# Kernel optimization log

Hardware: AMD Instinct MI355X
Metric: run time of the kernel (lower is better)

The kernel has to match this reference:

```python
import jax, jax.numpy as jnp
import numpy as np

N, S, P, F = 128, 32, 16, 256   # agents, samples, processes, encoder dim
H, NH = 4, 128                  # heads, n_hidden (is_concat=False -> n_hidden=out_features)
SLOPE = 0.2


def setup_inputs() -> dict:
    key = jax.random.key(0)
    k1, k2, k3, k4 = jax.random.split(key, 4)
    h = jax.random.normal(k1, (N, S, P, F), dtype=jnp.float32)
    W_l = jax.random.normal(k2, (F, H * NH), dtype=jnp.float32) / np.float32(np.sqrt(F))
    W_r = jax.random.normal(k3, (F, H * NH), dtype=jnp.float32) / np.float32(np.sqrt(F))
    attn_w = jax.random.normal(k4, (2 * NH,), dtype=jnp.float32) / np.float32(np.sqrt(2 * NH))
    return {"h": h, "W_l": W_l, "W_r": W_r, "attn_w": attn_w}


def reference(h, W_l, W_r, attn_w):
    n, s, p, f = h.shape
    hp = jnp.transpose(h, (1, 2, 0, 3))                 # [S,P,N,F]
    g_l = (hp @ W_l).reshape(s, p, n, H, NH)            # [S,P,N,H,NH]
    g_r = (hp @ W_r).reshape(s, p, n, H, NH)
    # attn(concat(gl[j], gr[i])) == <gl[j], a_l> + <gr[i], a_r>
    a_l, a_r = attn_w[:NH], attn_w[NH:]
    score_l = jnp.einsum('spnhf,f->spnh', g_l, a_l)     # contributes along j
    score_r = jnp.einsum('spnhf,f->spnh', g_r, a_r)     # contributes along i
    e = score_r[:, :, :, None, :] + score_l[:, :, None, :, :]   # [S,P,i,j,H]
    e = jnp.where(e >= 0, e, SLOPE * e)                 # LeakyReLU
    diag = jnp.eye(n, dtype=bool)[None, None, :, :, None]
    e = jnp.where(diag, -jnp.inf, e)                    # mask self-attention
    a = jax.nn.softmax(e, axis=3)                       # softmax over j
    out = jnp.einsum('spijh,spjhf->spihf', a, g_r)      # [S,P,N,H,NH]
    out = out.mean(axis=3)                              # is_concat=False -> mean over heads
    out = jnp.transpose(out, (2, 0, 1, 3))              # [N,S,P,NH]
    return out, a
```

## Files before the change

### kernel.cpp

```cpp
#include <hip/hip_runtime.h>
#include <hip/hip_bf16.h>

#define DI __device__ __forceinline__

namespace {
constexpr int N_ = 128, S_ = 32, P_ = 16, F_ = 256, H_ = 4, NH_ = 128;
constexpr int SP_ = S_ * P_;
constexpr int ROWS_ = N_ * SP_;
constexpr int GC_ = H_ * NH_;
constexpr float SLOPE_ = 0.2f;
constexpr int OUT_ELEMS = N_ * SP_ * NH_;
}

DI float lrelu(float x) { return x >= 0.f ? x : SLOPE_ * x; }

DI unsigned short f2h(float x) {
    _Float16 h = (_Float16)x;
    return __builtin_bit_cast(unsigned short, h);
}
DI float h2f(unsigned short b) {
    return (float)__builtin_bit_cast(_Float16, b);
}

typedef __fp16   fp16x2 __attribute__((ext_vector_type(2)));
typedef _Float16 f16x8 __attribute__((ext_vector_type(8)));
typedef float    f32x4 __attribute__((ext_vector_type(4)));

DI unsigned int pk2(float a, float b) {
    fp16x2 r = __builtin_amdgcn_cvt_pkrtz(a, b);
    return __builtin_bit_cast(unsigned int, r);
}

DI f32x4 mfma16h(uint4 a, uint4 b, f32x4 c) {
    return __builtin_amdgcn_mfma_f32_16x16x32_f16(
        __builtin_bit_cast(f16x8, a), __builtin_bit_cast(f16x8, b), c, 0, 0, 0);
}

__global__ __launch_bounds__(256) void prep_kernel(
    const float* __restrict__ Wl, const float* __restrict__ Wr,
    const float* __restrict__ aw, float* __restrict__ wls, float* __restrict__ wrs) {
    int t = blockIdx.x * 256 + threadIdx.x;
    int which = t >> 10;
    int f = (t & 1023) >> 2;
    int h = t & 3;
    const float* W = which ? Wr : Wl;
    const float* a = aw + which * NH_;
    const float* wrow = W + (size_t)f * GC_ + h * NH_;
    float s = 0.f;
    for (int k = 0; k < NH_; ++k) s += wrow[k] * a[k];
    (which ? wrs : wls)[f * H_ + h] = s;
}

__global__ __launch_bounds__(256) void prep_bt(
    const float* __restrict__ Wr, unsigned short* __restrict__ bth,
    unsigned short* __restrict__ btl) {
    int t = blockIdx.x * 256 + threadIdx.x;
    int col = t >> 5, k0 = (t & 31) * 8;
    union { unsigned short us[8]; uint4 v; } ph, pl;
#pragma unroll
    for (int e = 0; e < 8; ++e) {
        float v = Wr[(size_t)(k0 + e) * GC_ + col] * 256.0f;
        unsigned short hi = f2h(v);
        ph.us[e] = hi;
        pl.us[e] = f2h(v - h2f(hi));
    }
    *(uint4*)&bth[col * F_ + k0] = ph.v;
    *(uint4*)&btl[col * F_ + k0] = pl.v;
}

__global__ __launch_bounds__(256) void score_kernel(
    const float* __restrict__ hm, const float* __restrict__ wls,
    const float* __restrict__ wrs, float* __restrict__ sl, float* __restrict__ sr) {
    int r = blockIdx.x * 256 + threadIdx.x;
    const float4* hr  = (const float4*)(hm + (size_t)r * F_);
    const float4* wl4 = (const float4*)wls;
    const float4* wr4 = (const float4*)wrs;
    float4 al = {0.f,0.f,0.f,0.f}, ar = {0.f,0.f,0.f,0.f};
    for (int f0 = 0; f0 < F_; f0 += 4) {
        float4 hv = hr[f0 >> 2];
        float hx[4] = {hv.x, hv.y, hv.z, hv.w};
#pragma unroll
        for (int u = 0; u < 4; ++u) {
            float4 wl = wl4[f0 + u], wr = wr4[f0 + u];
            al.x += hx[u] * wl.x; al.y += hx[u] * wl.y;
            al.z += hx[u] * wl.z; al.w += hx[u] * wl.w;
            ar.x += hx[u] * wr.x; ar.y += hx[u] * wr.y;
            ar.z += hx[u] * wr.z; ar.w += hx[u] * wr.w;
        }
    }
    int n = r >> 9, sp = r & 511;
    ((float4*)sl)[sp * N_ + n] = al;
    ((float4*)sr)[sp * N_ + n] = ar;
}

__global__ __launch_bounds__(512, 2) void gat_fused(
    const float* __restrict__ sl_g, const float* __restrict__ sr_g,
    const float* __restrict__ hm,
    const unsigned short* __restrict__ bth, const unsigned short* __restrict__ btl,
    float* __restrict__ a_out, float* __restrict__ out) {
    constexpr int PA = 40;
    __shared__ __align__(16) unsigned char SMEM[141440];
    unsigned short* Ah0 = (unsigned short*)SMEM;
    unsigned short* Ah1 = Ah0 + 128 * PA;
    unsigned short* Al0 = Ah1 + 128 * PA;
    unsigned short* Al1 = Al0 + 128 * PA;
    unsigned short* gt4 = (unsigned short*)SMEM;
    float4* sl4   = (float4*)(SMEM + 131072);
    float4* sr4   = (float4*)(SMEM + 133120);
    float4* mrow4 = (float4*)(SMEM + 135168);
    float4* invs4 = (float4*)(SMEM + 137216);
    float*  slh   = (float*)(SMEM + 139264);
    float*  mx1   = (float*)(SMEM + 141376);
    float*  mx2   = (float*)(SMEM + 141392);
    int*    id1   = (int*)(SMEM + 141408);
    float* pm1 = (float*)mrow4;
    float* pm2 = pm1 + 128;
    int*   pid = (int*)(pm2 + 128);

    int sp = blockIdx.x;
    int t = threadIdx.x;
    int w = t >> 6, l = t & 63;
    int ls = l & 15, kg = l >> 4;

    if (t < 128) {
        float4 v = ((const float4*)sl_g)[sp * N_ + t];
        sl4[t] = v;
        slh[0 * 132 + t] = v.x; slh[1 * 132 + t] = v.y;
        slh[2 * 132 + t] = v.z; slh[3 * 132 + t] = v.w;
    } else if (t < 256) {
        sr4[t - 128] = ((const float4*)sr_g)[sp * N_ + (t - 128)];
    }
    __syncthreads();

    int arow = t >> 2, akc = (t & 3) * 8;
    const float* abase = hm + ((size_t)arow * 512 + sp) * 256 + akc;
    float4 s0 = *(const float4*)(abase);
    float4 s1 = *(const float4*)(abase + 4);

    if (t < 128) {
        int h = t >> 5, seg = t & 31;
        float m1 = -1e30f, m2 = -1e30f; int i1 = -1;
#pragma unroll
        for (int jj = 0; jj < 4; ++jj) {
            int j = seg * 4 + jj;
            float v = slh[h * 132 + j];
            if (v > m1) { m2 = m1; m1 = v; i1 = j; }
            else m2 = fmaxf(m2, v);
        }
        pm1[h * 32 + seg] = m1; pm2[h * 32 + seg] = m2; pid[h * 32 + seg] = i1;
    }
    __syncthreads();
    if (t < H_) {
        float m1 = -1e30f, m2 = -1e30f; int i1 = -1;
        for (int s = 0; s < 32; ++s) {
            float a1 = pm1[t * 32 + s], a2 = pm2[t * 32 + s]; int ai = pid[t * 32 + s];
            if (a1 > m1) { m2 = fmaxf(m1, a2); m1 = a1; i1 = ai; }
            else m2 = fmaxf(m2, a1);
        }
        mx1[t] = m1; mx2[t] = m2; id1[t] = i1;
    }
    __syncthreads();

    {
        float av[8] = {s0.x, s0.y, s0.z, s0.w, s1.x, s1.y, s1.z, s1.w};
        uint4 vh, vl;
        unsigned int* ph = (unsigned int*)&vh;
        unsigned int* pl = (unsigned int*)&vl;
#pragma unroll
        for (int e = 0; e < 8; e += 2) {
            unsigned int hp = pk2(av[e], av[e + 1]);
            float r0 = av[e]     - h2f((unsigned short)(hp & 0xffff));
            float r1 = av[e + 1] - h2f((unsigned short)(hp >> 16));
            ph[e >> 1] = hp;
            pl[e >> 1] = pk2(r0, r1);
        }
        *(uint4*)&Ah0[arow * PA + akc] = vh;
        *(uint4*)&Al0[arow * PA + akc] = vl;
    }

    int p1i = t & 127, p1h = t >> 7;
    float p1sri = ((const float*)&sr4[p1i])[p1h];
    float p1m = lrelu(p1sri + ((id1[p1h] == p1i) ? mx2[p1h] : mx1[p1h]));
    float p1sum = 0.f;

    __syncthreads();

    f32x4 acc[8][4];
#pragma unroll
    for (int m = 0; m < 8; ++m)
#pragma unroll
        for (int n = 0; n < 4; ++n) acc[m][n] = (f32x4){0.f, 0.f, 0.f, 0.f};

    for (int step = 0; step < 8; ++step) {
        unsigned short* AhC = (step & 1) ? Ah1 : Ah0;
        unsigned short* AlC = (step & 1) ? Al1 : Al0;
        unsigned short* AhN = (step & 1) ? Ah0 : Ah1;
        unsigned short* AlN = (step & 1) ? Al0 : Al1;
        float4 n0, n1;
        if (step < 7) {
            n0 = *(const float4*)(abase + (step + 1) * 32);
            n1 = *(const float4*)(abase + (step + 1) * 32 + 4);
        }
        int kglob = step * 32 + kg * 8;
        uint4 fbh[4], fbl[4];
#pragma unroll
        for (int n = 0; n < 4; ++n) {
            int c = n * 128 + w * 16 + ls;
            fbh[n] = *(const uint4*)&bth[(size_t)c * F_ + kglob];
            fbl[n] = *(const uint4*)&btl[(size_t)c * F_ + kglob];
        }
        {
            int j0 = step * 16;
#pragma unroll 4
            for (int j = j0; j < j0 + 16; ++j) {
                float e = lrelu(p1sri + slh[p1h * 132 + j]);
                float p = __expf(e - p1m);
                if (j != p1i) p1sum += p;
            }
            if (step == 7) {
                ((float*)&mrow4[p1i])[p1h] = p1m;
                ((float*)&invs4[p1i])[p1h] = 1.f / p1sum;
            }
        }
#pragma unroll
        for (int m = 0; m < 8; ++m) {
            int row = m * 16 + ls;
            uint4 fah = *(const uint4*)&AhC[row * PA + kg * 8];
            uint4 fal = *(const uint4*)&AlC[row * PA + kg * 8];
#pragma unroll
            for (int n = 0; n < 4; ++n) {
                acc[m][n] = mfma16h(fah, fbh[n], acc[m][n]);
                acc[m][n] = mfma16h(fah, fbl[n], acc[m][n]);
                acc[m][n] = mfma16h(fal, fbh[n], acc[m][n]);
            }
        }
        if (step < 7) {
            float av[8] = {n0.x, n0.y, n0.z, n0.w, n1.x, n1.y, n1.z, n1.w};
            uint4 vh, vl;
            unsigned int* ph = (unsigned int*)&vh;
            unsigned int* pl = (unsigned int*)&vl;
#pragma unroll
            for (int e = 0; e < 8; e += 2) {
                unsigned int hp = pk2(av[e], av[e + 1]);
                float r0 = av[e]     - h2f((unsigned short)(hp & 0xffff));
                float r1 = av[e + 1] - h2f((unsigned short)(hp >> 16));
                ph[e >> 1] = hp;
                pl[e >> 1] = pk2(r0, r1);
            }
            *(uint4*)&AhN[arow * PA + akc] = vh;
            *(uint4*)&AlN[arow * PA + akc] = vl;
        }
        __syncthreads();
    }

    int fl  = w * 16 + ls;
    int swz = (ls & 7) << 3;
    constexpr float gs = 0.00390625f;
#pragma unroll
    for (int m = 0; m < 8; ++m) {
        int nx = (m * 16 + kg * 4) ^ swz;
#pragma unroll
        for (int h = 0; h < H_; ++h) {
            uint2 pk;
            pk.x = pk2(acc[m][h][0] * gs, acc[m][h][1] * gs);
            pk.y = pk2(acc[m][h][2] * gs, acc[m][h][3] * gs);
            *(uint2*)&gt4[h * 16384 + fl * 128 + nx] = pk;
        }
    }
    __syncthreads();

    f32x4 aco[8];
#pragma unroll
    for (int n = 0; n < 8; ++n) aco[n] = (f32x4){0.f, 0.f, 0.f, 0.f};

    int i_my = w * 16 + ls;
    float4* a_base_g = (float4*)(a_out + (size_t)sp * 65536);
    int aj = t & 127, ib = t >> 7;
    float4 slv = sl4[aj];

    for (int h = 0; h < H_; ++h) {
        float sri = ((const float*)&sr4[i_my])[h];
        float mh  = ((const float*)&mrow4[i_my])[h];
        float sh  = ((const float*)&invs4[i_my])[h];
        uint4 pa[4];
#pragma unroll
        for (int k0i = 0; k0i < 4; ++k0i) {
            int jb = k0i * 32 + kg * 8;
            union { unsigned short us[8]; uint4 v; } pk;
#pragma unroll
            for (int e = 0; e < 8; ++e) {
                int j = jb + e;
                float p = (j == i_my) ? 0.f
                        : __expf(lrelu(sri + slh[h * 132 + j]) - mh) * sh;
                pk.us[e] = f2h(p);
            }
            pa[k0i] = pk.v;
        }
        __builtin_amdgcn_s_setprio(1);
#pragma unroll
        for (int k0i = 0; k0i < 4; ++k0i) {
            int koff = k0i * 32 + kg * 8;
#pragma unroll
            for (int n = 0; n < 8; ++n) {
                int f = n * 16 + ls;
                uint4 fb = *(const uint4*)&gt4[h * 16384 + f * 128 + (koff ^ swz)];
                aco[n] = mfma16h(pa[k0i], fb, aco[n]);
            }
        }
        __builtin_amdgcn_s_setprio(0);
#pragma unroll
        for (int q = 0; q < 8; ++q) {
            int i = h * 32 + q * 4 + ib;
            float4 srv = sr4[i], m4 = mrow4[i], s4 = invs4[i];
            float4 p;
            p.x = __expf(lrelu(srv.x + slv.x) - m4.x) * s4.x;
            p.y = __expf(lrelu(srv.y + slv.y) - m4.y) * s4.y;
            p.z = __expf(lrelu(srv.z + slv.z) - m4.z) * s4.z;
            p.w = __expf(lrelu(srv.w + slv.w) - m4.w) * s4.w;
            if (aj == i) { p.x = 0.f; p.y = 0.f; p.z = 0.f; p.w = 0.f; }
            a_base_g[i * N_ + aj] = p;
        }
    }

#pragma unroll
    for (int n = 0; n < 8; ++n) {
        int f = n * 16 + ls;
#pragma unroll
        for (int q = 0; q < 4; ++q)
            out[(size_t)(w * 16 + kg * 4 + q) * 65536 + (size_t)sp * NH_ + f] =
                aco[n][q] * 0.25f;
    }
}

extern "C" void kernel_launch(void* const* d_in, const int* in_sizes, int n_in,
                              void* d_out, int out_size, void* d_ws, size_t ws_size,
                              hipStream_t stream) {
    const float* hm = (const float*)d_in[0];
    const float* Wl = (const float*)d_in[1];
    const float* Wr = (const float*)d_in[2];
    const float* aw = (const float*)d_in[3];

    float* out   = (float*)d_out;
    float* a_out = out + OUT_ELEMS;

    char* ws = (char*)d_ws;
    float* sl  = (float*)ws;
    float* sr  = sl + SP_ * N_ * H_;
    float* wls = sr + SP_ * N_ * H_;
    float* wrs = wls + F_ * H_;
    unsigned short* bth = (unsigned short*)(wrs + F_ * H_);
    unsigned short* btl = bth + GC_ * F_;

    prep_kernel <<<8,           256, 0, stream>>>(Wl, Wr, aw, wls, wrs);
    prep_bt     <<<64,          256, 0, stream>>>(Wr, bth, btl);
    score_kernel<<<ROWS_ / 256, 256, 0, stream>>>(hm, wls, wrs, sl, sr);
    gat_fused   <<<SP_,         512, 0, stream>>>(sl, sr, hm, bth, btl, a_out, out);
}
```

Measured before the change: 133.5 us.

## Compute softmax sums in attention phase and write probabilities from MFMA fragments

Removes the separate softmax-denominator pass that ran during the projection GEMM loop and the separate recompute pass that wrote the attention matrix. Each thread now computes its row's exponentials once, reduces the sum with cross-lane shuffles, normalizes, and stores the probabilities directly while packing them for MFMA. This cuts exp work and shared memory, and drops one barrier. The cost is scattered 4-byte global stores with stride 4 instead of coalesced float4 stores. LeakyReLU also becomes a branch-free fmax.

```diff
diff --git a/kernel.cpp b/kernel.cpp
--- a/kernel.cpp
+++ b/kernel.cpp
@@ -12,7 +12,7 @@
 constexpr int OUT_ELEMS = N_ * SP_ * NH_;
 }
 
-DI float lrelu(float x) { return x >= 0.f ? x : SLOPE_ * x; }
+DI float lrelu(float x) { return fmaxf(x, SLOPE_ * x); }
 
 DI unsigned short f2h(float x) {
     _Float16 h = (_Float16)x;
@@ -99,23 +99,20 @@
     const unsigned short* __restrict__ bth, const unsigned short* __restrict__ btl,
     float* __restrict__ a_out, float* __restrict__ out) {
     constexpr int PA = 40;
-    __shared__ __align__(16) unsigned char SMEM[141440];
+    __shared__ __align__(16) unsigned char SMEM[136832];
     unsigned short* Ah0 = (unsigned short*)SMEM;
     unsigned short* Ah1 = Ah0 + 128 * PA;
     unsigned short* Al0 = Ah1 + 128 * PA;
     unsigned short* Al1 = Al0 + 128 * PA;
     unsigned short* gt4 = (unsigned short*)SMEM;
-    float4* sl4   = (float4*)(SMEM + 131072);
-    float4* sr4   = (float4*)(SMEM + 133120);
-    float4* mrow4 = (float4*)(SMEM + 135168);
-    float4* invs4 = (float4*)(SMEM + 137216);
-    float*  slh   = (float*)(SMEM + 139264);
-    float*  mx1   = (float*)(SMEM + 141376);
-    float*  mx2   = (float*)(SMEM + 141392);
-    int*    id1   = (int*)(SMEM + 141408);
-    float* pm1 = (float*)mrow4;
-    float* pm2 = pm1 + 128;
-    int*   pid = (int*)(pm2 + 128);
+    float4* sr4 = (float4*)(SMEM + 131072);
+    float*  slh = (float*)(SMEM + 133120);
+    float*  mx1 = (float*)(SMEM + 135232);
+    float*  mx2 = (float*)(SMEM + 135248);
+    int*    id1 = (int*)(SMEM + 135264);
+    float*  pm1 = (float*)(SMEM + 135280);
+    float*  pm2 = pm1 + 128;
+    int*    pid = (int*)(pm2 + 128);
 
     int sp = blockIdx.x;
     int t = threadIdx.x;
@@ -124,7 +121,6 @@
 
     if (t < 128) {
         float4 v = ((const float4*)sl_g)[sp * N_ + t];
-        sl4[t] = v;
         slh[0 * 132 + t] = v.x; slh[1 * 132 + t] = v.y;
         slh[2 * 132 + t] = v.z; slh[3 * 132 + t] = v.w;
     } else if (t < 256) {
@@ -159,7 +155,6 @@
         }
         mx1[t] = m1; mx2[t] = m2; id1[t] = i1;
     }
-    __syncthreads();
 
     {
         float av[8] = {s0.x, s0.y, s0.z, s0.w, s1.x, s1.y, s1.z, s1.w};
@@ -177,12 +172,6 @@
         *(uint4*)&Ah0[arow * PA + akc] = vh;
         *(uint4*)&Al0[arow * PA + akc] = vl;
     }
-
-    int p1i = t & 127, p1h = t >> 7;
-    float p1sri = ((const float*)&sr4[p1i])[p1h];
-    float p1m = lrelu(p1sri + ((id1[p1h] == p1i) ? mx2[p1h] : mx1[p1h]));
-    float p1sum = 0.f;
-
     __syncthreads();
 
     f32x4 acc[8][4];
@@ -209,19 +198,6 @@
             fbh[n] = *(const uint4*)&bth[(size_t)c * F_ + kglob];
             fbl[n] = *(const uint4*)&btl[(size_t)c * F_ + kglob];
         }
-        {
-            int j0 = step * 16;
-#pragma unroll 4
-            for (int j = j0; j < j0 + 16; ++j) {
-                float e = lrelu(p1sri + slh[p1h * 132 + j]);
-                float p = __expf(e - p1m);
-                if (j != p1i) p1sum += p;
-            }
-            if (step == 7) {
-                ((float*)&mrow4[p1i])[p1h] = p1m;
-                ((float*)&invs4[p1i])[p1h] = 1.f / p1sum;
-            }
-        }
 #pragma unroll
         for (int m = 0; m < 8; ++m) {
             int row = m * 16 + ls;
@@ -274,25 +250,41 @@
     for (int n = 0; n < 8; ++n) aco[n] = (f32x4){0.f, 0.f, 0.f, 0.f};
 
     int i_my = w * 16 + ls;
-    float4* a_base_g = (float4*)(a_out + (size_t)sp * 65536);
-    int aj = t & 127, ib = t >> 7;
-    float4 slv = sl4[aj];
+    float* a_irow = a_out + (size_t)sp * 65536 + (size_t)i_my * 512;
 
     for (int h = 0; h < H_; ++h) {
         float sri = ((const float*)&sr4[i_my])[h];
-        float mh  = ((const float*)&mrow4[i_my])[h];
-        float sh  = ((const float*)&invs4[i_my])[h];
-        uint4 pa[4];
+        float mh  = lrelu(sri + ((id1[h] == i_my) ? mx2[h] : mx1[h]));
+        float p[4][8];
+        float psum = 0.f;
 #pragma unroll
         for (int k0i = 0; k0i < 4; ++k0i) {
             int jb = k0i * 32 + kg * 8;
-            union { unsigned short us[8]; uint4 v; } pk;
+            float4 sa = *(const float4*)&slh[h * 132 + jb];
+            float4 sb = *(const float4*)&slh[h * 132 + jb + 4];
+            float sj[8] = {sa.x, sa.y, sa.z, sa.w, sb.x, sb.y, sb.z, sb.w};
 #pragma unroll
             for (int e = 0; e < 8; ++e) {
                 int j = jb + e;
-                float p = (j == i_my) ? 0.f
-                        : __expf(lrelu(sri + slh[h * 132 + j]) - mh) * sh;
-                pk.us[e] = f2h(p);
+                float v = (j == i_my) ? 0.f : __expf(lrelu(sri + sj[e]) - mh);
+                p[k0i][e] = v;
+                psum += v;
+            }
+        }
+        psum += __shfl_xor(psum, 16);
+        psum += __shfl_xor(psum, 32);
+        float sh = 1.f / psum;
+        uint4 pa[4];
+        float* a_h = a_irow + h;
+#pragma unroll
+        for (int k0i = 0; k0i < 4; ++k0i) {
+            union { unsigned short us[8]; uint4 v; } pk;
+            int jb = k0i * 32 + kg * 8;
+#pragma unroll
+            for (int e = 0; e < 8; ++e) {
+                float v = p[k0i][e] * sh;
+                a_h[(jb + e) * 4] = v;
+                pk.us[e] = f2h(v);
             }
             pa[k0i] = pk.v;
         }
@@ -308,18 +300,6 @@
             }
         }
         __builtin_amdgcn_s_setprio(0);
-#pragma unroll
-        for (int q = 0; q < 8; ++q) {
-            int i = h * 32 + q * 4 + ib;
-            float4 srv = sr4[i], m4 = mrow4[i], s4 = invs4[i];
-            float4 p;
-            p.x = __expf(lrelu(srv.x + slv.x) - m4.x) * s4.x;
-            p.y = __expf(lrelu(srv.y + slv.y) - m4.y) * s4.y;
-            p.z = __expf(lrelu(srv.z + slv.z) - m4.z) * s4.z;
-            p.w = __expf(lrelu(srv.w + slv.w) - m4.w) * s4.w;
-            if (aj == i) { p.x = 0.f; p.y = 0.f; p.z = 0.f; p.w = 0.f; }
-            a_base_g[i * N_ + aj] = p;
-        }
     }
 
 #pragma unroll
```

Result: slower. 239.9 us (+79.6%).

## Fuse score computation into main GAT kernel and merge prep kernels

Applied to the files above, without the earlier changes.

Removes the separate score_kernel, which re-read all of h from global memory, and computes the left/right attention scores inside gat_fused from the fp32 A-tile values already loaded for the MFMA projection. The two prep kernels are merged into one, cutting launches from four to two. Softmax max/sum computation moves out of the MFMA loop into a separate pass after the GEMM, so it no longer overlaps with MFMA work. Shared memory grows by about 8 KB, which may limit occupancy at 2 blocks per CU.

```diff
diff --git a/kernel.cpp b/kernel.cpp
--- a/kernel.cpp
+++ b/kernel.cpp
@@ -6,13 +6,12 @@
 namespace {
 constexpr int N_ = 128, S_ = 32, P_ = 16, F_ = 256, H_ = 4, NH_ = 128;
 constexpr int SP_ = S_ * P_;
-constexpr int ROWS_ = N_ * SP_;
 constexpr int GC_ = H_ * NH_;
 constexpr float SLOPE_ = 0.2f;
 constexpr int OUT_ELEMS = N_ * SP_ * NH_;
 }
 
-DI float lrelu(float x) { return x >= 0.f ? x : SLOPE_ * x; }
+DI float lrelu(float x) { return fmaxf(x, SLOPE_ * x); }
 
 DI unsigned short f2h(float x) {
     _Float16 h = (_Float16)x;
@@ -36,70 +35,44 @@
         __builtin_bit_cast(f16x8, a), __builtin_bit_cast(f16x8, b), c, 0, 0, 0);
 }
 
-__global__ __launch_bounds__(256) void prep_kernel(
+__global__ __launch_bounds__(256) void prep_all(
     const float* __restrict__ Wl, const float* __restrict__ Wr,
-    const float* __restrict__ aw, float* __restrict__ wls, float* __restrict__ wrs) {
+    const float* __restrict__ aw, float* __restrict__ wls, float* __restrict__ wrs,
+    unsigned short* __restrict__ bth, unsigned short* __restrict__ btl) {
     int t = blockIdx.x * 256 + threadIdx.x;
-    int which = t >> 10;
-    int f = (t & 1023) >> 2;
-    int h = t & 3;
-    const float* W = which ? Wr : Wl;
-    const float* a = aw + which * NH_;
-    const float* wrow = W + (size_t)f * GC_ + h * NH_;
-    float s = 0.f;
-    for (int k = 0; k < NH_; ++k) s += wrow[k] * a[k];
-    (which ? wrs : wls)[f * H_ + h] = s;
-}
-
-__global__ __launch_bounds__(256) void prep_bt(
-    const float* __restrict__ Wr, unsigned short* __restrict__ bth,
-    unsigned short* __restrict__ btl) {
-    int t = blockIdx.x * 256 + threadIdx.x;
-    int col = t >> 5, k0 = (t & 31) * 8;
-    union { unsigned short us[8]; uint4 v; } ph, pl;
-#pragma unroll
-    for (int e = 0; e < 8; ++e) {
-        float v = Wr[(size_t)(k0 + e) * GC_ + col] * 256.0f;
-        unsigned short hi = f2h(v);
-        ph.us[e] = hi;
-        pl.us[e] = f2h(v - h2f(hi));
-    }
-    *(uint4*)&bth[col * F_ + k0] = ph.v;
-    *(uint4*)&btl[col * F_ + k0] = pl.v;
-}
-
-__global__ __launch_bounds__(256) void score_kernel(
-    const float* __restrict__ hm, const float* __restrict__ wls,
-    const float* __restrict__ wrs, float* __restrict__ sl, float* __restrict__ sr) {
-    int r = blockIdx.x * 256 + threadIdx.x;
-    const float4* hr  = (const float4*)(hm + (size_t)r * F_);
-    const float4* wl4 = (const float4*)wls;
-    const float4* wr4 = (const float4*)wrs;
-    float4 al = {0.f,0.f,0.f,0.f}, ar = {0.f,0.f,0.f,0.f};
-    for (int f0 = 0; f0 < F_; f0 += 4) {
-        float4 hv = hr[f0 >> 2];
-        float hx[4] = {hv.x, hv.y, hv.z, hv.w};
-#pragma unroll
-        for (int u = 0; u < 4; ++u) {
-            float4 wl = wl4[f0 + u], wr = wr4[f0 + u];
-            al.x += hx[u] * wl.x; al.y += hx[u] * wl.y;
-            al.z += hx[u] * wl.z; al.w += hx[u] * wl.w;
-            ar.x += hx[u] * wr.x; ar.y += hx[u] * wr.y;
-            ar.z += hx[u] * wr.z; ar.w += hx[u] * wr.w;
-        }
-    }
-    int n = r >> 9, sp = r & 511;
-    ((float4*)sl)[sp * N_ + n] = al;
-    ((float4*)sr)[sp * N_ + n] = ar;
+    {
+        int col = t >> 5, k0 = (t & 31) * 8;
+        union { unsigned short us[8]; uint4 v; } ph, pl;
+#pragma unroll
+        for (int e = 0; e < 8; ++e) {
+            float v = Wr[(size_t)(k0 + e) * GC_ + col] * 256.0f;
+            unsigned short hi = f2h(v);
+            ph.us[e] = hi;
+            pl.us[e] = f2h(v - h2f(hi));
+        }
+        *(uint4*)&bth[col * F_ + k0] = ph.v;
+        *(uint4*)&btl[col * F_ + k0] = pl.v;
+    }
+    if (t < 2048) {
+        int which = t >> 10;
+        int f = (t & 1023) >> 2;
+        int h = t & 3;
+        const float* W = which ? Wr : Wl;
+        const float* a = aw + which * NH_;
+        const float* wrow = W + (size_t)f * GC_ + h * NH_;
+        float s = 0.f;
+        for (int k = 0; k < NH_; ++k) s += wrow[k] * a[k];
+        (which ? wrs : wls)[f * H_ + h] = s;
+    }
 }
 
 __global__ __launch_bounds__(512, 2) void gat_fused(
-    const float* __restrict__ sl_g, const float* __restrict__ sr_g,
     const float* __restrict__ hm,
     const unsigned short* __restrict__ bth, const unsigned short* __restrict__ btl,
+    const float* __restrict__ wls, const float* __restrict__ wrs,
     float* __restrict__ a_out, float* __restrict__ out) {
     constexpr int PA = 40;
-    __shared__ __align__(16) unsigned char SMEM[141440];
+    __shared__ __align__(16) unsigned char SMEM[149632];
     unsigned short* Ah0 = (unsigned short*)SMEM;
     unsigned short* Ah1 = Ah0 + 128 * PA;
     unsigned short* Al0 = Ah1 + 128 * PA;
@@ -110,9 +83,11 @@
     float4* mrow4 = (float4*)(SMEM + 135168);
     float4* invs4 = (float4*)(SMEM + 137216);
     float*  slh   = (float*)(SMEM + 139264);
-    float*  mx1   = (float*)(SMEM + 141376);
-    float*  mx2   = (float*)(SMEM + 141392);
-    int*    id1   = (int*)(SMEM + 141408);
+    float*  mx1   = (float*)(SMEM + 141392);
+    float*  mx2   = (float*)(SMEM + 141408);
+    int*    id1   = (int*)(SMEM + 141424);
+    float*  wlp   = (float*)(SMEM + 141440);
+    float*  wrp   = (float*)(SMEM + 145536);
     float* pm1 = (float*)mrow4;
     float* pm2 = pm1 + 128;
     int*   pid = (int*)(pm2 + 128);
@@ -122,44 +97,17 @@
     int w = t >> 6, l = t & 63;
     int ls = l & 15, kg = l >> 4;
 
-    if (t < 128) {
-        float4 v = ((const float4*)sl_g)[sp * N_ + t];
-        sl4[t] = v;
-        slh[0 * 132 + t] = v.x; slh[1 * 132 + t] = v.y;
-        slh[2 * 132 + t] = v.z; slh[3 * 132 + t] = v.w;
-    } else if (t < 256) {
-        sr4[t - 128] = ((const float4*)sr_g)[sp * N_ + (t - 128)];
-    }
-    __syncthreads();
+    if (t < 256)       *(float4*)&wlp[t * 4]         = ((const float4*)wls)[t];
+    else if (t < 512)  *(float4*)&wrp[(t - 256) * 4] = ((const float4*)wrs)[t - 256];
 
     int arow = t >> 2, akc = (t & 3) * 8;
     const float* abase = hm + ((size_t)arow * 512 + sp) * 256 + akc;
     float4 s0 = *(const float4*)(abase);
     float4 s1 = *(const float4*)(abase + 4);
-
-    if (t < 128) {
-        int h = t >> 5, seg = t & 31;
-        float m1 = -1e30f, m2 = -1e30f; int i1 = -1;
-#pragma unroll
-        for (int jj = 0; jj < 4; ++jj) {
-            int j = seg * 4 + jj;
-            float v = slh[h * 132 + j];
-            if (v > m1) { m2 = m1; m1 = v; i1 = j; }
-            else m2 = fmaxf(m2, v);
-        }
-        pm1[h * 32 + seg] = m1; pm2[h * 32 + seg] = m2; pid[h * 32 + seg] = i1;
-    }
-    __syncthreads();
-    if (t < H_) {
-        float m1 = -1e30f, m2 = -1e30f; int i1 = -1;
-        for (int s = 0; s < 32; ++s) {
-            float a1 = pm1[t * 32 + s], a2 = pm2[t * 32 + s]; int ai = pid[t * 32 + s];
-            if (a1 > m1) { m2 = fmaxf(m1, a2); m1 = a1; i1 = ai; }
-            else m2 = fmaxf(m2, a1);
-        }
-        mx1[t] = m1; mx2[t] = m2; id1[t] = i1;
-    }
-    __syncthreads();
+    __syncthreads();
+
+    float scl[4] = {0.f, 0.f, 0.f, 0.f};
+    float scr[4] = {0.f, 0.f, 0.f, 0.f};
 
     {
         float av[8] = {s0.x, s0.y, s0.z, s0.w, s1.x, s1.y, s1.z, s1.w};
@@ -176,13 +124,17 @@
         }
         *(uint4*)&Ah0[arow * PA + akc] = vh;
         *(uint4*)&Al0[arow * PA + akc] = vl;
-    }
-
-    int p1i = t & 127, p1h = t >> 7;
-    float p1sri = ((const float*)&sr4[p1i])[p1h];
-    float p1m = lrelu(p1sri + ((id1[p1h] == p1i) ? mx2[p1h] : mx1[p1h]));
-    float p1sum = 0.f;
-
+#pragma unroll
+        for (int e = 0; e < 8; ++e) {
+            int k = akc + e;
+            float4 wl = *(const float4*)&wlp[k * 4];
+            float4 wr = *(const float4*)&wrp[k * 4];
+            scl[0] += av[e] * wl.x; scl[1] += av[e] * wl.y;
+            scl[2] += av[e] * wl.z; scl[3] += av[e] * wl.w;
+            scr[0] += av[e] * wr.x; scr[1] += av[e] * wr.y;
+            scr[2] += av[e] * wr.z; scr[3] += av[e] * wr.w;
+        }
+    }
     __syncthreads();
 
     f32x4 acc[8][4];
@@ -209,19 +161,6 @@
             fbh[n] = *(const uint4*)&bth[(size_t)c * F_ + kglob];
             fbl[n] = *(const uint4*)&btl[(size_t)c * F_ + kglob];
         }
-        {
-            int j0 = step * 16;
-#pragma unroll 4
-            for (int j = j0; j < j0 + 16; ++j) {
-                float e = lrelu(p1sri + slh[p1h * 132 + j]);
-                float p = __expf(e - p1m);
-                if (j != p1i) p1sum += p;
-            }
-            if (step == 7) {
-                ((float*)&mrow4[p1i])[p1h] = p1m;
-                ((float*)&invs4[p1i])[p1h] = 1.f / p1sum;
-            }
-        }
 #pragma unroll
         for (int m = 0; m < 8; ++m) {
             int row = m * 16 + ls;
@@ -249,6 +188,17 @@
             }
             *(uint4*)&AhN[arow * PA + akc] = vh;
             *(uint4*)&AlN[arow * PA + akc] = vl;
+            int kb = (step + 1) * 32 + akc;
+#pragma unroll
+            for (int e = 0; e < 8; ++e) {
+                int k = kb + e;
+                float4 wl = *(const float4*)&wlp[k * 4];
+                float4 wr = *(const float4*)&wrp[k * 4];
+                scl[0] += av[e] * wl.x; scl[1] += av[e] * wl.y;
+                scl[2] += av[e] * wl.z; scl[3] += av[e] * wl.w;
+                scr[0] += av[e] * wr.x; scr[1] += av[e] * wr.y;
+                scr[2] += av[e] * wr.z; scr[3] += av[e] * wr.w;
+            }
         }
         __syncthreads();
     }
@@ -266,6 +216,60 @@
             pk.y = pk2(acc[m][h][2] * gs, acc[m][h][3] * gs);
             *(uint2*)&gt4[h * 16384 + fl * 128 + nx] = pk;
         }
+    }
+
+#pragma unroll
+    for (int h = 0; h < H_; ++h) {
+        scl[h] += __shfl_xor(scl[h], 1);
+        scl[h] += __shfl_xor(scl[h], 2);
+        scr[h] += __shfl_xor(scr[h], 1);
+        scr[h] += __shfl_xor(scr[h], 2);
+    }
+    if ((t & 3) == 0) {
+        int row = t >> 2;
+        sl4[row] = (float4){scl[0], scl[1], scl[2], scl[3]};
+        sr4[row] = (float4){scr[0], scr[1], scr[2], scr[3]};
+        slh[0 * 132 + row] = scl[0]; slh[1 * 132 + row] = scl[1];
+        slh[2 * 132 + row] = scl[2]; slh[3 * 132 + row] = scl[3];
+    }
+    __syncthreads();
+
+    if (t < 128) {
+        int h = t >> 5, seg = t & 31;
+        float m1 = -1e30f, m2 = -1e30f; int i1 = -1;
+#pragma unroll
+        for (int jj = 0; jj < 4; ++jj) {
+            int j = seg * 4 + jj;
+            float v = slh[h * 132 + j];
+            if (v > m1) { m2 = m1; m1 = v; i1 = j; }
+            else m2 = fmaxf(m2, v);
+        }
+        pm1[h * 32 + seg] = m1; pm2[h * 32 + seg] = m2; pid[h * 32 + seg] = i1;
+    }
+    __syncthreads();
+    if (t < H_) {
+        float m1 = -1e30f, m2 = -1e30f; int i1 = -1;
+        for (int s = 0; s < 32; ++s) {
+            float a1 = pm1[t * 32 + s], a2 = pm2[t * 32 + s]; int ai = pid[t * 32 + s];
+            if (a1 > m1) { m2 = fmaxf(m1, a2); m1 = a1; i1 = ai; }
+            else m2 = fmaxf(m2, a1);
+        }
+        mx1[t] = m1; mx2[t] = m2; id1[t] = i1;
+    }
+    __syncthreads();
+
+    {
+        int i = t & 127, h = t >> 7;
+        float sri = ((const float*)&sr4[i])[h];
+        float m = lrelu(sri + ((id1[h] == i) ? mx2[h] : mx1[h]));
+        float sum = 0.f;
+        for (int j = 0; j < N_; ++j) {
+            float e = lrelu(sri + slh[h * 132 + j]);
+            float p = __expf(e - m);
+            if (j != i) sum += p;
+        }
+        ((float*)&mrow4[i])[h] = m;
+        ((float*)&invs4[i])[h] = 1.f / sum;
     }
     __syncthreads();
 
@@ -344,15 +348,11 @@
     float* a_out = out + OUT_ELEMS;
 
     char* ws = (char*)d_ws;
-    float* sl  = (float*)ws;
-    float* sr  = sl + SP_ * N_ * H_;
-    float* wls = sr + SP_ * N_ * H_;
+    float* wls = (float*)ws;
     float* wrs = wls + F_ * H_;
     unsigned short* bth = (unsigned short*)(wrs + F_ * H_);
     unsigned short* btl = bth + GC_ * F_;
 
-    prep_kernel <<<8,           256, 0, stream>>>(Wl, Wr, aw, wls, wrs);
-    prep_bt     <<<64,          256, 0, stream>>>(Wr, bth, btl);
-    score_kernel<<<ROWS_ / 256, 256, 0, stream>>>(hm, wls, wrs, sl, sr);
-    gat_fused   <<<SP_,         512, 0, stream>>>(sl, sr, hm, bth, btl, a_out, out);
-}
+    prep_all  <<<64,  256, 0, stream>>>(Wl, Wr, aw, wls, wrs, bth, btl);
+    gat_fused <<<SP_, 512, 0, stream>>>(hm, bth, btl, wls, wrs, a_out, out);
+}
```

After: 154.5 us. 1.16x slower.
